# Optimization experiments

Hardware: AMD Instinct MI355X
Metric: run time of the kernel (lower is better)

## Reference

```python
import jax, jax.numpy as jnp
import numpy as np

N = 50000      # nodes
E = 800000     # edges
IN = 64        # in_channels
HID = 256      # hidden_dim
LAT = 64       # latent_dim
KS = 2         # kernel_size per dim
DIM = 3        # pseudo-coordinate dim
K = KS ** DIM  # 8 spline weight matrices


def spline_basis_coeffs(pseudo, ks, dim, dtype):
    """Degree-1 open B-spline basis: returns per-edge coefficients c [E, ks**dim]."""
    e = pseudo.shape[0]
    v = pseudo * (ks - 1)                                   # [E, dim]
    bot = jnp.clip(jnp.floor(v), 0, ks - 1).astype(jnp.int32)
    frac = v - bot
    c = jnp.zeros((e, ks ** dim), dtype)
    rows = jnp.arange(e)
    for s in range(2 ** dim):  # 8 knot combinations (fixed small loop)
        w = jnp.ones(e, dtype)
        idx = jnp.zeros(e, jnp.int32)
        for d in range(dim):
            bit = (s >> d) & 1
            w = w * (frac[:, d] if bit else 1.0 - frac[:, d])
            idx = idx + jnp.clip(bot[:, d] + bit, 0, ks - 1) * (ks ** d)
        c = c.at[rows, idx].add(w)
    return c


def spline_conv(x, edge_index, pseudo, W, Wroot, b):
    """SplineConv with aggr='mean', root weight and bias (degree-1 open splines)."""
    src, dst = edge_index[0], edge_index[1]
    n = x.shape[0]
    e = pseudo.shape[0]
    c = spline_basis_coeffs(pseudo, KS, DIM, x.dtype)        # [E, K]
    x_src = x[src]                                           # [E, in] gather
    deg = jax.ops.segment_sum(jnp.ones(e, x.dtype), dst, num_segments=n)
    inv_deg = (1.0 / jnp.maximum(deg, 1.0))[:, None]         # [N, 1] mean aggr
    out = jnp.zeros((n, W.shape[2]), x.dtype)
    for k in range(W.shape[0]):  # K=8 fixed loop; scatter-add then dense matmul
        agg = jax.ops.segment_sum(c[:, k:k + 1] * x_src, dst, num_segments=n)
        out = out + (agg * inv_deg) @ W[k]
    return out + x @ Wroot + b


def setup_inputs() -> dict:
    key = jax.random.key(0)
    ks = jax.random.split(key, 12)
    x = jax.random.normal(ks[0], (N, IN), jnp.float32)
    edge_index = jax.random.randint(ks[1], (2, E), 0, N, jnp.int32)
    s = 0.05
    return {
        "x": x,
        "edge_index": edge_index,
        "conv1_W": jax.random.normal(ks[2], (K, IN, HID), jnp.float32) * s,
        "conv1_root": jax.random.normal(ks[3], (IN, HID), jnp.float32) * s,
        "conv1_b": jnp.zeros((HID,), jnp.float32),
        "conv2_W": jax.random.normal(ks[4], (K, HID, LAT), jnp.float32) * s,
        "conv2_root": jax.random.normal(ks[5], (HID, LAT), jnp.float32) * s,
        "conv2_b": jnp.zeros((LAT,), jnp.float32),
        "dec_w1": jax.random.normal(ks[6], (LAT, HID), jnp.float32) * s,
        "dec_b1": jnp.zeros((HID,), jnp.float32),
        "dec_w2": jax.random.normal(ks[7], (HID, IN), jnp.float32) * s,
        "dec_b2": jnp.zeros((IN,), jnp.float32),
    }


def reference(x, edge_index, conv1_W, conv1_root, conv1_b,
              conv2_W, conv2_root, conv2_b,
              dec_w1, dec_b1, dec_w2, dec_b2):
    pseudo = jnp.zeros((edge_index.shape[1], DIM), x.dtype)  # forward builds zeros
    h = jax.nn.relu(spline_conv(x, edge_index, pseudo, conv1_W, conv1_root, conv1_b))
    z = spline_conv(h, edge_index, pseudo, conv2_W, conv2_root, conv2_b)
    h2 = jax.nn.relu(z @ dec_w1 + dec_b1)
    return h2 @ dec_w2 + dec_b2
```

## Files before the change

### kernel.cpp

```cpp
#include <hip/hip_runtime.h>
#include <hip/hip_bf16.h>


#define THREADS 256

typedef __attribute__((ext_vector_type(8))) short bf16x8;
typedef __attribute__((ext_vector_type(4))) float f32x4;

__device__ __forceinline__ float bf2f(unsigned short u) {
    unsigned v = ((unsigned)u) << 16;
    return __builtin_bit_cast(float, v);
}
__device__ __forceinline__ unsigned short f2bf(float f) {
    __hip_bfloat16 h = __float2bfloat16(f);
    return __builtin_bit_cast(unsigned short, h);
}
__device__ __forceinline__ void acc4(float* f, uint2 v) {
    f[0] += bf2f((unsigned short)v.x);
    f[1] += bf2f((unsigned short)(v.x >> 16));
    f[2] += bf2f((unsigned short)v.y);
    f[3] += bf2f((unsigned short)(v.y >> 16));
}

__device__ __forceinline__ void pack_one(unsigned short* dst,
                                         const float* W0, const float* W1,
                                         int NB, int ksplit, int colsplit,
                                         int ld0, int ld1, int t) {
    int i = t & 7, lane = (t >> 3) & 63, rest = t >> 9;
    int j = rest % NB, s = rest / NB;
    int k = s * 32 + ((lane >> 4) << 3) + i;
    int c = (j << 4) + (lane & 15);
    float v;
    if (c >= colsplit)    v = W1[(size_t)k * ld1 + (c - colsplit)];
    else if (k >= ksplit) v = W1[(size_t)(k - ksplit) * ld1 + c];
    else                  v = W0[(size_t)k * ld0 + c];
    dst[t] = f2bf(v);
}

#define BIG (1 << 30)

__global__ void prep_kernel(const float* __restrict__ W1g, const float* __restrict__ root1,
                            const float* __restrict__ W2g, const float* __restrict__ root2,
                            const float* __restrict__ dw1, const float* __restrict__ dw2,
                            const float* __restrict__ x, const int* __restrict__ dstv,
                            int* __restrict__ bcnt,
                            unsigned short* __restrict__ Pb1,
                            unsigned short* __restrict__ Pb2,
                            unsigned short* __restrict__ Pd1,
                            unsigned short* __restrict__ Pd2,
                            unsigned short* __restrict__ xb,
                            int n, int E, int pb_pack) {
    if ((int)blockIdx.x >= pb_pack) {
        __shared__ int hist[256];
        int t = threadIdx.x;
        hist[t] = 0;
        __syncthreads();
        int e0 = ((int)blockIdx.x - pb_pack) * 4096;
#pragma unroll
        for (int i = 0; i < 16; ++i) {
            int e = e0 + t + i * 256;
            if (e < E) atomicAdd(&hist[dstv[e] >> 8], 1);
        }
        __syncthreads();
        int h = hist[t];
        if (h) atomicAdd(&bcnt[t], h);
        return;
    }
    int t = blockIdx.x * blockDim.x + threadIdx.x;
    if (t < 32768) {
        pack_one(Pb1, W1g, root1, 16, 64, BIG, 256, 256, t);
    } else if (t < 65536) {
        pack_one(Pb2, W2g, root2, 8, BIG, 64, 64, 64, t - 32768);
    } else if (t < 81920) {
        pack_one(Pd1, dw1, dw1, 16, BIG, BIG, 256, 256, t - 65536);
    } else if (t < 98304) {
        pack_one(Pd2, dw2, dw2, 4, BIG, BIG, 64, 64, t - 81920);
    } else if (t < 98304 + n * 16) {
        int u = t - 98304;
        int row = u >> 4, c4 = (u & 15) * 4;
        float4 v = *(const float4*)(x + (size_t)row * 64 + c4);
        unsigned lo = (unsigned)f2bf(v.x) | ((unsigned)f2bf(v.y) << 16);
        unsigned hi = (unsigned)f2bf(v.z) | ((unsigned)f2bf(v.w) << 16);
        uint2 o; o.x = lo; o.y = hi;
        *(uint2*)(xb + (size_t)row * 64 + c4) = o;
    }
}

__global__ __launch_bounds__(256) void partition_edges(
    const int* __restrict__ src, const int* __restrict__ dst,
    const int* __restrict__ bcnt, int* __restrict__ bcur,
    int* __restrict__ epack, int E) {
    __shared__ int hist[256];
    __shared__ int base[256];
    __shared__ int lcur[256];
    __shared__ int bb[256];
    int t = threadIdx.x;
    hist[t] = 0;
    __syncthreads();
    int e0 = blockIdx.x * 4096;
    int myd[16], mys[16];
#pragma unroll
    for (int i = 0; i < 16; ++i) {
        int e = e0 + t + i * 256;
        int d = (e < E) ? dst[e] : -1;
        mys[i] = (e < E) ? src[e] : 0;
        myd[i] = d;
        if (d >= 0) atomicAdd(&hist[d >> 8], 1);
    }
    int cb = bcnt[t];
    bb[t] = cb;
    __syncthreads();
    for (int off = 1; off < 256; off <<= 1) {
        int xv = (t >= off) ? bb[t - off] : 0;
        __syncthreads();
        bb[t] += xv;
        __syncthreads();
    }
    int bbase_t = bb[t] - cb;
    int h = hist[t];
    if (h > 0) base[t] = bbase_t + atomicAdd(&bcur[t], h);
    lcur[t] = 0;
    __syncthreads();
#pragma unroll
    for (int i = 0; i < 16; ++i) {
        int d = myd[i];
        if (d >= 0) {
            int b = d >> 8;
            int p = atomicAdd(&lcur[b], 1);
            epack[base[b] + p] = ((d & 255) << 20) | mys[i];
        }
    }
}

__global__ __launch_bounds__(256) void bucket_fill2(
    const int* __restrict__ epack, const int* __restrict__ bcnt,
    int* __restrict__ offs, float* __restrict__ invd,
    int* __restrict__ esrc, int N) {
    __shared__ int sb_[256];
    __shared__ int nh[256];
    __shared__ int loff[256];
    __shared__ int ncur[256];
    __shared__ int stage[8192];
    int b = blockIdx.x, t = threadIdx.x;
    int n0 = b << 8;
    int cntn = min(256, N - n0);
    int cb = bcnt[t];
    sb_[t] = cb;
    __syncthreads();
    for (int off = 1; off < 256; off <<= 1) {
        int xv = (t >= off) ? sb_[t - off] : 0;
        __syncthreads();
        sb_[t] += xv;
        __syncthreads();
    }
    int ebase = b ? sb_[b - 1] : 0;
    int ecount = sb_[b] - ebase;
    if (b == 0 && t == 0) offs[N] = sb_[255];
    nh[t] = 0;
    __syncthreads();
    for (int i = t; i < ecount; i += 256)
        atomicAdd(&nh[epack[ebase + i] >> 20], 1);
    __syncthreads();
    int v = nh[t];
    loff[t] = v;
    __syncthreads();
    for (int off = 1; off < 256; off <<= 1) {
        int xv = (t >= off) ? loff[t - off] : 0;
        __syncthreads();
        loff[t] += xv;
        __syncthreads();
    }
    int ex = loff[t] - v;
    loff[t] = ex;
    if (t < cntn) {
        offs[n0 + t] = ebase + ex;
        invd[n0 + t] = 1.0f / (float)max(v, 1);
    }
    ncur[t] = 0;
    __syncthreads();
    bool useLds = (ecount <= 8192);
    for (int i = t; i < ecount; i += 256) {
        int p = epack[ebase + i];
        int dl = p >> 20;
        int pos = atomicAdd(&ncur[dl], 1);
        int g = loff[dl] + pos;
        int sv = p & 0xFFFFF;
        if (useLds) stage[g] = sv;
        else        esrc[ebase + g] = sv;
    }
    __syncthreads();
    if (useLds)
        for (int i = t; i < ecount; i += 256) esrc[ebase + i] = stage[i];
}

__global__ void agg_x4(const unsigned short* __restrict__ xb,
                       unsigned short* __restrict__ agg1,
                       const int* __restrict__ esrc, const int* __restrict__ offs,
                       const float* __restrict__ invd, int n) {
    int node = blockIdx.x * 4 + (threadIdx.x >> 6);
    if (node >= n) return;
    int l = threadIdx.x & 63;
    int slot = l >> 4, c = l & 15;
    const unsigned short* tb = xb + c * 4;
    int s = offs[node], e = offs[node + 1];
    float a0[4] = {}, a1[4] = {}, a2[4] = {}, a3[4] = {};
    int j = s;
    for (; j + 16 <= e; j += 16) {
        int i0 = esrc[j + slot],      i1 = esrc[j + 4 + slot];
        int i2 = esrc[j + 8 + slot],  i3 = esrc[j + 12 + slot];
        uint2 v0 = *(const uint2*)(tb + (size_t)i0 * 64);
        uint2 v1 = *(const uint2*)(tb + (size_t)i1 * 64);
        uint2 v2 = *(const uint2*)(tb + (size_t)i2 * 64);
        uint2 v3 = *(const uint2*)(tb + (size_t)i3 * 64);
        acc4(a0, v0); acc4(a1, v1); acc4(a2, v2); acc4(a3, v3);
    }
    for (; j + 4 <= e; j += 4) {
        uint2 v0 = *(const uint2*)(tb + (size_t)esrc[j + slot] * 64);
        acc4(a0, v0);
    }
    if (slot < e - j) {
        uint2 v0 = *(const uint2*)(tb + (size_t)esrc[j + slot] * 64);
        acc4(a1, v0);
    }
    float r[4];
#pragma unroll
    for (int k = 0; k < 4; ++k) {
        r[k] = (a0[k] + a1[k]) + (a2[k] + a3[k]);
        r[k] += __shfl_xor(r[k], 16);
        r[k] += __shfl_xor(r[k], 32);
    }
    if (slot == 0) {
        float iv = invd[node];
        unsigned lo = (unsigned)f2bf(r[0] * iv) | ((unsigned)f2bf(r[1] * iv) << 16);
        unsigned hi = (unsigned)f2bf(r[2] * iv) | ((unsigned)f2bf(r[3] * iv) << 16);
        uint2 o; o.x = lo; o.y = hi;
        *(uint2*)(agg1 + (size_t)node * 64 + c * 4) = o;
    }
}

__global__ void agg_z4(const unsigned short* __restrict__ hw,
                       const unsigned short* __restrict__ hroot,
                       const int* __restrict__ esrc, const int* __restrict__ offs,
                       const float* __restrict__ invd, const float* __restrict__ b2,
                       unsigned short* __restrict__ z, int n) {
    int node = blockIdx.x * 4 + (threadIdx.x >> 6);
    if (node >= n) return;
    int l = threadIdx.x & 63;
    int slot = l >> 4, c = l & 15;
    const unsigned short* tb = hw + c * 4;
    int s = offs[node], e = offs[node + 1];
    float a0[4] = {}, a1[4] = {}, a2[4] = {}, a3[4] = {};
    int j = s;
    for (; j + 16 <= e; j += 16) {
        int i0 = esrc[j + slot],      i1 = esrc[j + 4 + slot];
        int i2 = esrc[j + 8 + slot],  i3 = esrc[j + 12 + slot];
        uint2 v0 = *(const uint2*)(tb + (size_t)i0 * 64);
        uint2 v1 = *(const uint2*)(tb + (size_t)i1 * 64);
        uint2 v2 = *(const uint2*)(tb + (size_t)i2 * 64);
        uint2 v3 = *(const uint2*)(tb + (size_t)i3 * 64);
        acc4(a0, v0); acc4(a1, v1); acc4(a2, v2); acc4(a3, v3);
    }
    for (; j + 4 <= e; j += 4) {
        uint2 v0 = *(const uint2*)(tb + (size_t)esrc[j + slot] * 64);
        acc4(a0, v0);
    }
    if (slot < e - j) {
        uint2 v0 = *(const uint2*)(tb + (size_t)esrc[j + slot] * 64);
        acc4(a1, v0);
    }
    float r[4];
#pragma unroll
    for (int k = 0; k < 4; ++k) {
        r[k] = (a0[k] + a1[k]) + (a2[k] + a3[k]);
        r[k] += __shfl_xor(r[k], 16);
        r[k] += __shfl_xor(r[k], 32);
    }
    if (slot == 0) {
        float iv = invd[node];
        uint2 hr = *(const uint2*)(hroot + (size_t)node * 64 + c * 4);
        float v0 = r[0] * iv + bf2f((unsigned short)hr.x) + b2[c * 4 + 0];
        float v1 = r[1] * iv + bf2f((unsigned short)(hr.x >> 16)) + b2[c * 4 + 1];
        float v2 = r[2] * iv + bf2f((unsigned short)hr.y) + b2[c * 4 + 2];
        float v3 = r[3] * iv + bf2f((unsigned short)(hr.y >> 16)) + b2[c * 4 + 3];
        unsigned lo = (unsigned)f2bf(v0) | ((unsigned)f2bf(v1) << 16);
        unsigned hi = (unsigned)f2bf(v2) | ((unsigned)f2bf(v3) << 16);
        uint2 o; o.x = lo; o.y = hi;
        *(uint2*)(z + (size_t)node * 64 + c * 4) = o;
    }
}

template <int K1, int NBW2, bool SPLITA, bool OUTFP32>
__global__ __launch_bounds__(256) void gemm_fused(
    const unsigned short* __restrict__ A0, const unsigned short* __restrict__ A1,
    const unsigned short* __restrict__ Bp1, const float* __restrict__ bias1,
    const unsigned short* __restrict__ Bp2, const float* __restrict__ bias2,
    void* __restrict__ out0, unsigned short* __restrict__ out1, int n)
{
    constexpr int KS1 = K1 / 32;
    constexpr int NB2 = NBW2 * 4;
    __shared__ unsigned short ht[64][264];

    const int m0 = blockIdx.x * 64;
    const int lane = threadIdx.x & 63;
    const int w = threadIdx.x >> 6;
    const int quad = lane >> 4;
    const int l16 = lane & 15;

    {
        f32x4 acc[4][4] = {};
        for (int s = 0; s < KS1; ++s) {
            const unsigned short* tab;
            int ks;
            if (SPLITA && s >= KS1 / 2) { tab = A1; ks = s - KS1 / 2; }
            else                        { tab = A0; ks = s; }
            const unsigned short* Arow = tab + (size_t)(m0 + l16) * 64 + ks * 32 + quad * 8;
            bf16x8 a[4];
#pragma unroll
            for (int mb = 0; mb < 4; ++mb)
                a[mb] = *(const bf16x8*)(Arow + (size_t)mb * 16 * 64);
#pragma unroll
            for (int jn = 0; jn < 4; ++jn) {
                int j = w * 4 + jn;
                bf16x8 b = *(const bf16x8*)(Bp1 + ((size_t)(s * 16 + j) * 64 + lane) * 8);
#pragma unroll
                for (int mb = 0; mb < 4; ++mb)
                    acc[mb][jn] = __builtin_amdgcn_mfma_f32_16x16x32_bf16(a[mb], b, acc[mb][jn], 0, 0, 0);
            }
        }
#pragma unroll
        for (int jn = 0; jn < 4; ++jn) {
            int col = (w * 4 + jn) * 16 + l16;
            float bv = bias1[col];
#pragma unroll
            for (int mb = 0; mb < 4; ++mb)
#pragma unroll
                for (int r = 0; r < 4; ++r) {
                    int row = mb * 16 + quad * 4 + r;
                    ht[row][col] = f2bf(fmaxf(acc[mb][jn][r] + bv, 0.f));
                }
        }
    }
    __syncthreads();

    {
        f32x4 acc[4][NBW2] = {};
        for (int s = 0; s < 8; ++s) {
            bf16x8 a[4];
#pragma unroll
            for (int mb = 0; mb < 4; ++mb)
                a[mb] = *(const bf16x8*)&ht[mb * 16 + l16][s * 32 + quad * 8];
#pragma unroll
            for (int jn = 0; jn < NBW2; ++jn) {
                int j = w * NBW2 + jn;
                bf16x8 b = *(const bf16x8*)(Bp2 + ((size_t)(s * NB2 + j) * 64 + lane) * 8);
#pragma unroll
                for (int mb = 0; mb < 4; ++mb)
                    acc[mb][jn] = __builtin_amdgcn_mfma_f32_16x16x32_bf16(a[mb], b, acc[mb][jn], 0, 0, 0);
            }
        }
#pragma unroll
        for (int jn = 0; jn < NBW2; ++jn) {
            int col = (w * NBW2 + jn) * 16 + l16;
            float bv = (OUTFP32 && bias2) ? bias2[col] : 0.f;
#pragma unroll
            for (int mb = 0; mb < 4; ++mb)
#pragma unroll
                for (int r = 0; r < 4; ++r) {
                    int row = m0 + mb * 16 + quad * 4 + r;
                    if (row < n) {
                        float v = acc[mb][jn][r] + bv;
                        if (OUTFP32) {
                            ((float*)out0)[(size_t)row * 64 + col] = v;
                        } else if (col < 64) {
                            ((unsigned short*)out0)[(size_t)row * 64 + col] = f2bf(v);
                        } else {
                            out1[(size_t)row * 64 + (col - 64)] = f2bf(v);
                        }
                    }
                }
        }
    }
}

extern "C" void kernel_launch(void* const* d_in, const int* in_sizes, int n_in,
                              void* d_out, int out_size, void* d_ws, size_t ws_size,
                              hipStream_t stream) {
    const float* x      = (const float*)d_in[0];
    const int*   ei     = (const int*)d_in[1];
    const float* W1g    = (const float*)d_in[2];
    const float* root1  = (const float*)d_in[3];
    const float* b1     = (const float*)d_in[4];
    const float* W2g    = (const float*)d_in[5];
    const float* root2  = (const float*)d_in[6];
    const float* b2     = (const float*)d_in[7];
    const float* dw1    = (const float*)d_in[8];
    const float* db1    = (const float*)d_in[9];
    const float* dw2    = (const float*)d_in[10];
    const float* db2    = (const float*)d_in[11];
    float* out = (float*)d_out;

    const int N = in_sizes[0] / 64;
    const int E = in_sizes[1] / 2;
    const int Npad = N + 64;
    const int* srcv = ei;
    const int* dstv = ei + E;

    char* ws = (char*)d_ws;
    auto alloc = [&](size_t bytes) -> void* {
        void* p = (void*)ws;
        ws += (bytes + 255) & ~(size_t)255;
        return p;
    };
    int*   bcnt   = (int*)alloc(1024);
    int*   bcur   = (int*)alloc(1024);
    int*   offs   = (int*)alloc((size_t)(N + 1) * 4);
    float* invd   = (float*)alloc((size_t)N * 4);
    int*   esrc   = (int*)alloc((size_t)E * 4);
    int*   epack  = (int*)alloc((size_t)E * 4);
    unsigned short* Pb1 = (unsigned short*)alloc(32768 * 2);
    unsigned short* Pb2 = (unsigned short*)alloc(32768 * 2);
    unsigned short* Pd1 = (unsigned short*)alloc(16384 * 2);
    unsigned short* Pd2 = (unsigned short*)alloc(16384 * 2);
    unsigned short* xb    = (unsigned short*)alloc((size_t)Npad * 64 * 2);
    unsigned short* agg1  = (unsigned short*)alloc((size_t)Npad * 64 * 2);
    unsigned short* hw    = (unsigned short*)alloc((size_t)Npad * 64 * 2);
    unsigned short* hroot = (unsigned short*)alloc((size_t)Npad * 64 * 2);
    unsigned short* z     = (unsigned short*)alloc((size_t)Npad * 64 * 2);

    hipMemsetAsync(bcnt, 0, 2048, stream);

    int gb = (N + 63) / 64;
    int nbkt = (N + 255) / 256;
    int pa = (E + 4095) / 4096;
    int pb_pack = (98304 + N * 16 + THREADS - 1) / THREADS;

    prep_kernel<<<pb_pack + pa, THREADS, 0, stream>>>(
        W1g, root1, W2g, root2, dw1, dw2, x, dstv, bcnt,
        Pb1, Pb2, Pd1, Pd2, xb, N, E, pb_pack);
    partition_edges<<<pa, 256, 0, stream>>>(srcv, dstv, bcnt, bcur, epack, E);
    bucket_fill2<<<nbkt, 256, 0, stream>>>(epack, bcnt, offs, invd, esrc, N);

    agg_x4<<<(N + 3) / 4, THREADS, 0, stream>>>(xb, agg1, esrc, offs, invd, N);
    gemm_fused<128, 2, true, false><<<gb, 256, 0, stream>>>(
        agg1, xb, Pb1, b1, Pb2, nullptr, hw, hroot, N);
    agg_z4<<<(N + 3) / 4, THREADS, 0, stream>>>(hw, hroot, esrc, offs, invd, b2, z, N);
    gemm_fused<64, 1, false, true><<<gb, 256, 0, stream>>>(
        z, nullptr, Pd1, db1, Pd2, db2, out, nullptr, N);
}
```

Measured before the change: 212.8 us.

## Split neighbor aggregation into two source-half passes for gather cache locality

```diff
diff --git a/kernel.cpp b/kernel.cpp
--- a/kernel.cpp
+++ b/kernel.cpp
@@ -134,12 +134,14 @@
 
 __global__ __launch_bounds__(256) void bucket_fill2(
     const int* __restrict__ epack, const int* __restrict__ bcnt,
-    int* __restrict__ offs, float* __restrict__ invd,
-    int* __restrict__ esrc, int N) {
+    int* __restrict__ offs, int* __restrict__ moffs, float* __restrict__ invd,
+    int* __restrict__ esrc, int N, int Nhalf) {
     __shared__ int sb_[256];
     __shared__ int nh[256];
+    __shared__ int nlo[256];
     __shared__ int loff[256];
-    __shared__ int ncur[256];
+    __shared__ int nclo[256];
+    __shared__ int nchi[256];
     __shared__ int stage[8192];
     int b = blockIdx.x, t = threadIdx.x;
     int n0 = b << 8;
@@ -157,9 +159,14 @@
     int ecount = sb_[b] - ebase;
     if (b == 0 && t == 0) offs[N] = sb_[255];
     nh[t] = 0;
-    __syncthreads();
-    for (int i = t; i < ecount; i += 256)
-        atomicAdd(&nh[epack[ebase + i] >> 20], 1);
+    nlo[t] = 0;
+    __syncthreads();
+    for (int i = t; i < ecount; i += 256) {
+        int p = epack[ebase + i];
+        int dl = p >> 20, sv = p & 0xFFFFF;
+        atomicAdd(&nh[dl], 1);
+        if (sv < Nhalf) atomicAdd(&nlo[dl], 1);
+    }
     __syncthreads();
     int v = nh[t];
     loff[t] = v;
@@ -174,17 +181,19 @@
     loff[t] = ex;
     if (t < cntn) {
         offs[n0 + t] = ebase + ex;
+        moffs[n0 + t] = ebase + ex + nlo[t];
         invd[n0 + t] = 1.0f / (float)max(v, 1);
     }
-    ncur[t] = 0;
+    nclo[t] = 0;
+    nchi[t] = 0;
     __syncthreads();
     bool useLds = (ecount <= 8192);
     for (int i = t; i < ecount; i += 256) {
         int p = epack[ebase + i];
-        int dl = p >> 20;
-        int pos = atomicAdd(&ncur[dl], 1);
+        int dl = p >> 20, sv = p & 0xFFFFF;
+        int pos = (sv < Nhalf) ? atomicAdd(&nclo[dl], 1)
+                               : nlo[dl] + atomicAdd(&nchi[dl], 1);
         int g = loff[dl] + pos;
-        int sv = p & 0xFFFFF;
         if (useLds) stage[g] = sv;
         else        esrc[ebase + g] = sv;
     }
@@ -193,16 +202,20 @@
         for (int i = t; i < ecount; i += 256) esrc[ebase + i] = stage[i];
 }
 
-__global__ void agg_x4(const unsigned short* __restrict__ xb,
-                       unsigned short* __restrict__ agg1,
-                       const int* __restrict__ esrc, const int* __restrict__ offs,
-                       const float* __restrict__ invd, int n) {
+template <bool FIRST, bool ZEPI>
+__global__ void agg_pass(const unsigned short* __restrict__ tab,
+                         const unsigned short* __restrict__ hroot,
+                         const int* __restrict__ esrc,
+                         const int* __restrict__ sa, const int* __restrict__ ea,
+                         const float* __restrict__ invd, const float* __restrict__ b2,
+                         float* __restrict__ P, unsigned short* __restrict__ outb,
+                         int n) {
     int node = blockIdx.x * 4 + (threadIdx.x >> 6);
     if (node >= n) return;
     int l = threadIdx.x & 63;
     int slot = l >> 4, c = l & 15;
-    const unsigned short* tb = xb + c * 4;
-    int s = offs[node], e = offs[node + 1];
+    const unsigned short* tb = tab + c * 4;
+    int s = sa[node], e = ea[node];
     float a0[4] = {}, a1[4] = {}, a2[4] = {}, a3[4] = {};
     int j = s;
     for (; j + 16 <= e; j += 16) {
@@ -230,62 +243,28 @@
         r[k] += __shfl_xor(r[k], 32);
     }
     if (slot == 0) {
-        float iv = invd[node];
-        unsigned lo = (unsigned)f2bf(r[0] * iv) | ((unsigned)f2bf(r[1] * iv) << 16);
-        unsigned hi = (unsigned)f2bf(r[2] * iv) | ((unsigned)f2bf(r[3] * iv) << 16);
-        uint2 o; o.x = lo; o.y = hi;
-        *(uint2*)(agg1 + (size_t)node * 64 + c * 4) = o;
-    }
-}
-
-__global__ void agg_z4(const unsigned short* __restrict__ hw,
-                       const unsigned short* __restrict__ hroot,
-                       const int* __restrict__ esrc, const int* __restrict__ offs,
-                       const float* __restrict__ invd, const float* __restrict__ b2,
-                       unsigned short* __restrict__ z, int n) {
-    int node = blockIdx.x * 4 + (threadIdx.x >> 6);
-    if (node >= n) return;
-    int l = threadIdx.x & 63;
-    int slot = l >> 4, c = l & 15;
-    const unsigned short* tb = hw + c * 4;
-    int s = offs[node], e = offs[node + 1];
-    float a0[4] = {}, a1[4] = {}, a2[4] = {}, a3[4] = {};
-    int j = s;
-    for (; j + 16 <= e; j += 16) {
-        int i0 = esrc[j + slot],      i1 = esrc[j + 4 + slot];
-        int i2 = esrc[j + 8 + slot],  i3 = esrc[j + 12 + slot];
-        uint2 v0 = *(const uint2*)(tb + (size_t)i0 * 64);
-        uint2 v1 = *(const uint2*)(tb + (size_t)i1 * 64);
-        uint2 v2 = *(const uint2*)(tb + (size_t)i2 * 64);
-        uint2 v3 = *(const uint2*)(tb + (size_t)i3 * 64);
-        acc4(a0, v0); acc4(a1, v1); acc4(a2, v2); acc4(a3, v3);
-    }
-    for (; j + 4 <= e; j += 4) {
-        uint2 v0 = *(const uint2*)(tb + (size_t)esrc[j + slot] * 64);
-        acc4(a0, v0);
-    }
-    if (slot < e - j) {
-        uint2 v0 = *(const uint2*)(tb + (size_t)esrc[j + slot] * 64);
-        acc4(a1, v0);
-    }
-    float r[4];
-#pragma unroll
-    for (int k = 0; k < 4; ++k) {
-        r[k] = (a0[k] + a1[k]) + (a2[k] + a3[k]);
-        r[k] += __shfl_xor(r[k], 16);
-        r[k] += __shfl_xor(r[k], 32);
-    }
-    if (slot == 0) {
-        float iv = invd[node];
-        uint2 hr = *(const uint2*)(hroot + (size_t)node * 64 + c * 4);
-        float v0 = r[0] * iv + bf2f((unsigned short)hr.x) + b2[c * 4 + 0];
-        float v1 = r[1] * iv + bf2f((unsigned short)(hr.x >> 16)) + b2[c * 4 + 1];
-        float v2 = r[2] * iv + bf2f((unsigned short)hr.y) + b2[c * 4 + 2];
-        float v3 = r[3] * iv + bf2f((unsigned short)(hr.y >> 16)) + b2[c * 4 + 3];
-        unsigned lo = (unsigned)f2bf(v0) | ((unsigned)f2bf(v1) << 16);
-        unsigned hi = (unsigned)f2bf(v2) | ((unsigned)f2bf(v3) << 16);
-        uint2 o; o.x = lo; o.y = hi;
-        *(uint2*)(z + (size_t)node * 64 + c * 4) = o;
+        if (FIRST) {
+            float4 o; o.x = r[0]; o.y = r[1]; o.z = r[2]; o.w = r[3];
+            *(float4*)(P + (size_t)node * 64 + c * 4) = o;
+        } else {
+            float4 p = *(const float4*)(P + (size_t)node * 64 + c * 4);
+            r[0] += p.x; r[1] += p.y; r[2] += p.z; r[3] += p.w;
+            float iv = invd[node];
+            float v0, v1, v2, v3;
+            if (ZEPI) {
+                uint2 hr = *(const uint2*)(hroot + (size_t)node * 64 + c * 4);
+                v0 = r[0] * iv + bf2f((unsigned short)hr.x) + b2[c * 4 + 0];
+                v1 = r[1] * iv + bf2f((unsigned short)(hr.x >> 16)) + b2[c * 4 + 1];
+                v2 = r[2] * iv + bf2f((unsigned short)hr.y) + b2[c * 4 + 2];
+                v3 = r[3] * iv + bf2f((unsigned short)(hr.y >> 16)) + b2[c * 4 + 3];
+            } else {
+                v0 = r[0] * iv; v1 = r[1] * iv; v2 = r[2] * iv; v3 = r[3] * iv;
+            }
+            unsigned lo = (unsigned)f2bf(v0) | ((unsigned)f2bf(v1) << 16);
+            unsigned hi = (unsigned)f2bf(v2) | ((unsigned)f2bf(v3) << 16);
+            uint2 o; o.x = lo; o.y = hi;
+            *(uint2*)(outb + (size_t)node * 64 + c * 4) = o;
+        }
     }
 }
 
@@ -402,6 +381,7 @@
     const int N = in_sizes[0] / 64;
     const int E = in_sizes[1] / 2;
     const int Npad = N + 64;
+    const int Nhalf = N / 2;
     const int* srcv = ei;
     const int* dstv = ei + E;
 
@@ -414,6 +394,7 @@
     int*   bcnt   = (int*)alloc(1024);
     int*   bcur   = (int*)alloc(1024);
     int*   offs   = (int*)alloc((size_t)(N + 1) * 4);
+    int*   moffs  = (int*)alloc((size_t)N * 4);
     float* invd   = (float*)alloc((size_t)N * 4);
     int*   esrc   = (int*)alloc((size_t)E * 4);
     int*   epack  = (int*)alloc((size_t)E * 4);
@@ -426,24 +407,32 @@
     unsigned short* hw    = (unsigned short*)alloc((size_t)Npad * 64 * 2);
     unsigned short* hroot = (unsigned short*)alloc((size_t)Npad * 64 * 2);
     unsigned short* z     = (unsigned short*)alloc((size_t)Npad * 64 * 2);
+    float* Ppart = (float*)alloc((size_t)Npad * 64 * 4);
 
     hipMemsetAsync(bcnt, 0, 2048, stream);
 
     int gb = (N + 63) / 64;
     int nbkt = (N + 255) / 256;
     int pa = (E + 4095) / 4096;
+    int gg = (N + 3) / 4;
     int pb_pack = (98304 + N * 16 + THREADS - 1) / THREADS;
 
     prep_kernel<<<pb_pack + pa, THREADS, 0, stream>>>(
         W1g, root1, W2g, root2, dw1, dw2, x, dstv, bcnt,
         Pb1, Pb2, Pd1, Pd2, xb, N, E, pb_pack);
     partition_edges<<<pa, 256, 0, stream>>>(srcv, dstv, bcnt, bcur, epack, E);
-    bucket_fill2<<<nbkt, 256, 0, stream>>>(epack, bcnt, offs, invd, esrc, N);
-
-    agg_x4<<<(N + 3) / 4, THREADS, 0, stream>>>(xb, agg1, esrc, offs, invd, N);
+    bucket_fill2<<<nbkt, 256, 0, stream>>>(epack, bcnt, offs, moffs, invd, esrc, N, Nhalf);
+
+    agg_pass<true, false><<<gg, THREADS, 0, stream>>>(
+        xb, nullptr, esrc, offs, moffs, invd, nullptr, Ppart, nullptr, N);
+    agg_pass<false, false><<<gg, THREADS, 0, stream>>>(
+        xb, nullptr, esrc, moffs, offs + 1, invd, nullptr, Ppart, agg1, N);
     gemm_fused<128, 2, true, false><<<gb, 256, 0, stream>>>(
         agg1, xb, Pb1, b1, Pb2, nullptr, hw, hroot, N);
-    agg_z4<<<(N + 3) / 4, THREADS, 0, stream>>>(hw, hroot, esrc, offs, invd, b2, z, N);
+    agg_pass<true, false><<<gg, THREADS, 0, stream>>>(
+        hw, nullptr, esrc, offs, moffs, invd, nullptr, Ppart, nullptr, N);
+    agg_pass<false, true><<<gg, THREADS, 0, stream>>>(
+        hw, hroot, esrc, moffs, offs + 1, invd, b2, Ppart, z, N);
     gemm_fused<64, 1, false, true><<<gb, 256, 0, stream>>>(
         z, nullptr, Pd1, db1, Pd2, db2, out, nullptr, N);
 }
```

Measured after the change: 244.9 us. 15.1% more time.
